# Kernel tuning notes

Measured on AMD Instinct MI355X. Metric: run time of the kernel, lower is better.

## Reference

```python
import jax, jax.numpy as jnp
import numpy as np

B, N, DIM = 2, 2048, 1024
H, DH = 16, 64
NNK = 2          # num_null_kv
SCALE = 8.0
LN_EPS = 1e-5
L2_EPS = 1e-12


def layer_norm(x, gamma):
    mu = jnp.mean(x, axis=-1, keepdims=True)
    var = jnp.var(x, axis=-1, keepdims=True)
    return (x - mu) * jax.lax.rsqrt(var + LN_EPS) * gamma  # beta buffer is zeros


def l2norm(t):
    n = jnp.sqrt(jnp.sum(t * t, axis=-1, keepdims=True))
    return t / jnp.maximum(n, L2_EPS)


def setup_inputs() -> dict:
    key = jax.random.key(0)
    ks = jax.random.split(key, 9)
    x = jax.random.normal(ks[0], (B, N, DIM), dtype=jnp.float32)
    mask = jax.random.randint(ks[1], (B, N), 0, 2).astype(bool)
    attn_bias = jax.random.normal(ks[2], (H, N, N), dtype=jnp.float32)
    gamma = jnp.ones((DIM,), dtype=jnp.float32)
    null_kv = jax.random.normal(ks[3], (H, 2 * NNK, DH), dtype=jnp.float32)
    Wq = jax.random.normal(ks[4], (DIM, H * DH), dtype=jnp.float32) * 0.02
    Wkv = jax.random.normal(ks[5], (DIM, 2 * H * DH), dtype=jnp.float32) * 0.02
    q_scale = jnp.ones((DH,), dtype=jnp.float32)
    k_scale = jnp.ones((DH,), dtype=jnp.float32)
    Wo = jax.random.normal(ks[6], (H * DH, DIM), dtype=jnp.float32) * 0.02
    return {"x": x, "mask": mask, "attn_bias": attn_bias, "gamma": gamma,
            "null_kv": null_kv, "Wq": Wq, "Wkv": Wkv,
            "q_scale": q_scale, "k_scale": k_scale, "Wo": Wo}


def reference(x, mask, attn_bias, gamma, null_kv, Wq, Wkv, q_scale, k_scale, Wo):
    b, n, dim = x.shape
    h, dh = null_kv.shape[0], null_kv.shape[-1]
    # NOTE: in the original module kv_input is captured BEFORE self.norm(x),
    # so k/v come from the un-normalized x (context=None path).
    kv_input = x
    xn = layer_norm(x, gamma)
    q = (xn @ Wq).reshape(b, n, h, dh).transpose(0, 2, 1, 3)          # b h n d
    kv = (kv_input @ Wkv).reshape(b, n, 2, h, dh)
    k = kv[:, :, 0].transpose(0, 2, 1, 3)                              # b h n d
    v = kv[:, :, 1].transpose(0, 2, 1, 3)                              # b h n d
    # null kv: 'h (n r) d -> h n r d', unbind r
    nkv = null_kv.reshape(h, NNK, 2, dh)
    nk = jnp.broadcast_to(nkv[:, :, 0][None], (b, h, NNK, dh))
    nv = jnp.broadcast_to(nkv[:, :, 1][None], (b, h, NNK, dh))
    k = jnp.concatenate([nk, k], axis=-2)                              # b h j d
    v = jnp.concatenate([nv, v], axis=-2)
    q = l2norm(q) * q_scale
    k = l2norm(k) * k_scale
    sim = jnp.einsum('bhid,bhjd->bhij', q, k) * SCALE                  # b h i j
    i, j = sim.shape[-2], sim.shape[-1]
    # attn_bias padded with num_null_kv zeros on the left of last dim
    bias = jnp.pad(attn_bias, ((0, 0), (0, 0), (NNK, 0)))
    sim = sim + bias[None]                                             # broadcast over batch
    neg = -jnp.finfo(sim.dtype).max
    # key padding mask, null kv always attendable
    m = jnp.pad(mask, ((0, 0), (NNK, 0)), constant_values=True)       # b j
    sim = jnp.where(m[:, None, None, :], sim, neg)
    # causal mask with diagonal offset j - i + 1 (null tokens always visible)
    causal = jnp.triu(jnp.ones((i, j), dtype=bool), k=j - i + 1)
    sim = jnp.where(causal, neg, sim)
    attn = jax.nn.softmax(sim, axis=-1)
    out = jnp.einsum('bhij,bhjd->bhid', attn, v)
    out = out.transpose(0, 2, 1, 3).reshape(b, n, h * dh)
    return out @ Wo
```

## Files before the change

kernel.cpp:

```cpp
#include <hip/hip_runtime.h>
#include <math.h>

typedef unsigned short ushort_t;
typedef __attribute__((ext_vector_type(8))) short bf16x8_t;
typedef __attribute__((ext_vector_type(4))) float floatx4;

typedef __attribute__((address_space(3))) unsigned int lds_uint;
typedef const __attribute__((address_space(1))) unsigned int glob_uint;

__device__ inline void gl_lds16(const ushort_t* g, ushort_t* l) {
    __builtin_amdgcn_global_load_lds((glob_uint*)g, (lds_uint*)l, 16, 0, 0);
}

__device__ inline float bf2f(ushort_t u) {
    return __uint_as_float(((unsigned int)u) << 16);
}
__device__ inline ushort_t f2bf(float f) {
    unsigned int u = __float_as_uint(f);
    unsigned int r = (u + 0x7fffu + ((u >> 16) & 1u)) >> 16;
    return (ushort_t)r;
}
__device__ inline float wave_sum(float v) {
    #pragma unroll
    for (int m = 1; m < 64; m <<= 1) v += __shfl_xor(v, m, 64);
    return v;
}

__global__ __launch_bounds__(256) void transpose_split(const float* __restrict__ W,
                                                       ushort_t* __restrict__ WTh,
                                                       ushort_t* __restrict__ WTl,
                                                       int K, int N) {
    __shared__ float t[32][33];
    int n0 = blockIdx.x * 32, k0 = blockIdx.y * 32;
    int tx = threadIdx.x, ty = threadIdx.y;
    for (int i = ty; i < 32; i += 8)
        t[i][tx] = W[(size_t)(k0 + i) * N + n0 + tx];
    __syncthreads();
    for (int i = ty; i < 32; i += 8) {
        float v = t[tx][i];
        ushort_t hv = f2bf(v);
        size_t o = (size_t)(n0 + i) * K + k0 + tx;
        WTh[o] = hv;
        WTl[o] = f2bf(v - bf2f(hv));
    }
}

__global__ __launch_bounds__(256) void ln_split(const float* __restrict__ x,
                                                const float* __restrict__ gamma,
                                                ushort_t* __restrict__ xnh,
                                                ushort_t* __restrict__ xnl,
                                                ushort_t* __restrict__ xh,
                                                ushort_t* __restrict__ xl) {
    int row = blockIdx.x, tid = threadIdx.x;
    int wid = tid >> 6, lane = tid & 63;
    float v[4];
    float s1 = 0.f, s2 = 0.f;
    #pragma unroll
    for (int i = 0; i < 4; ++i) {
        v[i] = x[(size_t)row * 1024 + tid + 256 * i];
        s1 += v[i];
        s2 += v[i] * v[i];
    }
    s1 = wave_sum(s1);
    s2 = wave_sum(s2);
    __shared__ float red[8];
    if (lane == 0) { red[wid] = s1; red[4 + wid] = s2; }
    __syncthreads();
    float S1 = red[0] + red[1] + red[2] + red[3];
    float S2 = red[4] + red[5] + red[6] + red[7];
    float mu = S1 * (1.0f / 1024.0f);
    float var = S2 * (1.0f / 1024.0f) - mu * mu;
    float rs = 1.0f / sqrtf(var + 1e-5f);
    #pragma unroll
    for (int i = 0; i < 4; ++i) {
        int c = tid + 256 * i;
        size_t o = (size_t)row * 1024 + c;
        ushort_t hx = f2bf(v[i]);
        xh[o] = hx;
        xl[o] = f2bf(v[i] - bf2f(hx));
        float xnv = (v[i] - mu) * rs * gamma[c];
        ushort_t hn = f2bf(xnv);
        xnh[o] = hn;
        xnl[o] = f2bf(xnv - bf2f(hn));
    }
}

__global__ __launch_bounds__(256) void gemm_bf3(const ushort_t* __restrict__ Ah,
                                                const ushort_t* __restrict__ Al,
                                                const ushort_t* __restrict__ Bh,
                                                const ushort_t* __restrict__ Bl,
                                                float* __restrict__ C,
                                                int M, int N, int K) {
    __shared__ ushort_t As[128 * 64];
    __shared__ ushort_t Bs[128 * 64];
    int tid = threadIdx.x;
    int w = tid >> 6, lane = tid & 63;
    int wm = w >> 1, wn = w & 1;
    int row0 = blockIdx.y * 128, col0 = blockIdx.x * 128;
    int l15 = lane & 15, l4 = lane >> 4;
    int rx = l15 & 7;
    floatx4 acc[4][4];
    #pragma unroll
    for (int i = 0; i < 4; ++i)
        #pragma unroll
        for (int j = 0; j < 4; ++j)
            #pragma unroll
            for (int v = 0; v < 4; ++v) acc[i][j][v] = 0.f;

    int nk = K >> 5;
    for (int kt = 0; kt < nk; ++kt) {
        __syncthreads();
        #pragma unroll
        for (int c = 0; c < 4; ++c) {
            int idx = c * 256 + tid;
            int r = idx >> 3, cl = idx & 7;
            int cg = cl ^ (r & 7);
            const ushort_t* ga = (cg < 4 ? Ah : Al)
                + (size_t)(row0 + r) * K + kt * 32 + (cg & 3) * 8;
            gl_lds16(ga, &As[(c * 256 + w * 64) * 8]);
            const ushort_t* gb = (cg < 4 ? Bh : Bl)
                + (size_t)(col0 + r) * K + kt * 32 + (cg & 3) * 8;
            gl_lds16(gb, &Bs[(c * 256 + w * 64) * 8]);
        }
        __syncthreads();
        bf16x8_t af_h[4], af_l[4], bf_h[4], bf_l[4];
        #pragma unroll
        for (int mi = 0; mi < 4; ++mi) {
            int r = wm * 64 + mi * 16 + l15;
            af_h[mi] = *(const bf16x8_t*)&As[(r * 8 + (l4 ^ rx)) * 8];
            af_l[mi] = *(const bf16x8_t*)&As[(r * 8 + ((4 + l4) ^ rx)) * 8];
        }
        #pragma unroll
        for (int ni = 0; ni < 4; ++ni) {
            int r = wn * 64 + ni * 16 + l15;
            bf_h[ni] = *(const bf16x8_t*)&Bs[(r * 8 + (l4 ^ rx)) * 8];
            bf_l[ni] = *(const bf16x8_t*)&Bs[(r * 8 + ((4 + l4) ^ rx)) * 8];
        }
        #pragma unroll
        for (int mi = 0; mi < 4; ++mi)
            #pragma unroll
            for (int ni = 0; ni < 4; ++ni) {
                acc[mi][ni] = __builtin_amdgcn_mfma_f32_16x16x32_bf16(
                    af_h[mi], bf_h[ni], acc[mi][ni], 0, 0, 0);
                acc[mi][ni] = __builtin_amdgcn_mfma_f32_16x16x32_bf16(
                    af_h[mi], bf_l[ni], acc[mi][ni], 0, 0, 0);
                acc[mi][ni] = __builtin_amdgcn_mfma_f32_16x16x32_bf16(
                    af_l[mi], bf_h[ni], acc[mi][ni], 0, 0, 0);
            }
    }
    #pragma unroll
    for (int mi = 0; mi < 4; ++mi)
        #pragma unroll
        for (int ni = 0; ni < 4; ++ni)
            #pragma unroll
            for (int v = 0; v < 4; ++v) {
                int rr = row0 + wm * 64 + mi * 16 + l4 * 4 + v;
                int cc = col0 + wn * 64 + ni * 16 + l15;
                C[(size_t)rr * N + cc] = acc[mi][ni][v];
            }
}

__global__ __launch_bounds__(256) void l2scale_q(const float* __restrict__ q,
                                                 const float* __restrict__ qs,
                                                 ushort_t* __restrict__ Qh,
                                                 ushort_t* __restrict__ Ql) {
    int rid = blockIdx.x * 4 + (threadIdx.x >> 6);
    int lane = threadIdx.x & 63;
    int h = rid & 15, n = (rid >> 4) & 2047, b = rid >> 15;
    float v = q[(size_t)rid * 64 + lane];
    float nrm = sqrtf(wave_sum(v * v));
    float qn = v / fmaxf(nrm, 1e-12f) * qs[lane] * 8.0f;
    size_t o = (((size_t)(b * 16 + h)) * 2048 + n) * 64 + lane;
    ushort_t hv = f2bf(qn);
    Qh[o] = hv;
    Ql[o] = f2bf(qn - bf2f(hv));
}

__global__ __launch_bounds__(256) void build_kv(const float* __restrict__ kv,
                                                const float* __restrict__ nullkv,
                                                const float* __restrict__ ks,
                                                ushort_t* __restrict__ Kh,
                                                ushort_t* __restrict__ Kl,
                                                ushort_t* __restrict__ VTh) {
    __shared__ ushort_t Vt[64][72];
    int tid = threadIdx.x;
    int w = tid >> 6, lane = tid & 63;
    int bh = blockIdx.y, b = bh >> 4, h = bh & 15;
    int j0 = blockIdx.x * 64;
    for (int jj = 0; jj < 16; ++jj) {
        int jl = w * 16 + jj;
        int j = j0 + jl;
        float kf = 0.f, vf = 0.f;
        if (j < 2) {
            kf = nullkv[(h * 4 + 2 * j) * 64 + lane];
            vf = nullkv[(h * 4 + 2 * j + 1) * 64 + lane];
        } else if (j < 2050) {
            int n = j - 2;
            size_t base = ((size_t)b * 2048 + n) * 2048;
            kf = kv[base + h * 64 + lane];
            vf = kv[base + 1024 + h * 64 + lane];
        }
        float nrm = sqrtf(wave_sum(kf * kf));
        float kn = (j < 2050) ? kf / fmaxf(nrm, 1e-12f) * ks[lane] : 0.f;
        size_t o = ((size_t)bh * 2112 + j) * 64 + lane;
        ushort_t khv = f2bf(kn);
        Kh[o] = khv;
        Kl[o] = f2bf(kn - bf2f(khv));
        Vt[jl][lane] = f2bf(vf);
    }
    __syncthreads();
    int d = tid >> 2, seg = tid & 3;
    ushort_t buf[16];
    #pragma unroll
    for (int e = 0; e < 16; ++e) buf[e] = Vt[seg * 16 + e][d];
    size_t o = ((size_t)bh * 64 + d) * 2112 + j0 + seg * 16;
    *(bf16x8_t*)&VTh[o]     = *(const bf16x8_t*)&buf[0];
    *(bf16x8_t*)&VTh[o + 8] = *(const bf16x8_t*)&buf[8];
}

__global__ __launch_bounds__(256) void attn_mfma(const ushort_t* __restrict__ Qh,
                                                 const ushort_t* __restrict__ Ql,
                                                 const ushort_t* __restrict__ Kh,
                                                 const ushort_t* __restrict__ Kl,
                                                 const ushort_t* __restrict__ VTh,
                                                 const float* __restrict__ bias,
                                                 const int* __restrict__ mask,
                                                 ushort_t* __restrict__ aoh,
                                                 ushort_t* __restrict__ aol) {
    __shared__ ushort_t Ks[2][64 * 128];
    __shared__ ushort_t Vs[2][64 * 64];
    __shared__ ushort_t Ps[4][16 * 72];

    int tid = threadIdx.x;
    int w = tid >> 6, lane = tid & 63;
    int quad = lane >> 4, l15 = lane & 15;
    int rx = l15 & 7;
    int qt = 31 - blockIdx.x;
    int bh = blockIdx.y;
    int b = bh >> 4, h = bh & 15;
    int i0 = qt * 64, r0 = i0 + w * 16;
    const int nIter = qt + 2;

    auto stage = [&](int j0, ushort_t* kd, ushort_t* vd) {
        #pragma unroll
        for (int c = 0; c < 4; ++c) {
            int idx = c * 256 + tid;
            int r = idx >> 4, cl = idx & 15;
            int cg = (cl & 8) | ((cl ^ (r & 7)) & 7);
            const ushort_t* g = ((cg & 8) ? Kl : Kh)
                + ((size_t)bh * 2112 + j0 + r) * 64 + (cg & 7) * 8;
            gl_lds16(g, &kd[(c * 256 + w * 64) * 8]);
        }
        #pragma unroll
        for (int c = 0; c < 2; ++c) {
            int idx = c * 256 + tid;
            int r = idx >> 3, cl = idx & 7;
            int cg = cl ^ (r & 7);
            const ushort_t* g = VTh + ((size_t)bh * 64 + r) * 2112 + j0 + cg * 8;
            gl_lds16(g, &vd[(c * 256 + w * 64) * 8]);
        }
    };

    float bv_n[4][4];
    int km_n[4];
    auto prefetchB = [&](int j0n) {
        #pragma unroll
        for (int jt = 0; jt < 4; ++jt) {
            int jg = j0n + jt * 16 + l15;
            km_n[jt] = (jg < 2) ? 1 : (jg < 2050 ? mask[b * 2048 + jg - 2] : 0);
            #pragma unroll
            for (int reg = 0; reg < 4; ++reg) {
                int ig = r0 + quad * 4 + reg;
                bv_n[jt][reg] = (jg >= 2 && jg < 2050)
                    ? bias[((size_t)h * 2048 + ig) * 2048 + (jg - 2)] : 0.f;
            }
        }
    };

    stage(0, Ks[0], Vs[0]);
    prefetchB(0);

    bf16x8_t aqh[2], aql[2];
    {
        size_t qbase = ((size_t)bh * 2048 + r0 + l15) * 64 + quad * 8;
        aqh[0] = *(const bf16x8_t*)&Qh[qbase];
        aqh[1] = *(const bf16x8_t*)&Qh[qbase + 32];
        aql[0] = *(const bf16x8_t*)&Ql[qbase];
        aql[1] = *(const bf16x8_t*)&Ql[qbase + 32];
    }

    floatx4 o_acc[4];
    float l_acc[4];
    #pragma unroll
    for (int dt = 0; dt < 4; ++dt)
        #pragma unroll
        for (int v = 0; v < 4; ++v) o_acc[dt][v] = 0.f;
    #pragma unroll
    for (int r = 0; r < 4; ++r) l_acc[r] = 0.f;

    __syncthreads();

    for (int it = 0; it < nIter; ++it) {
        int cur = it & 1;
        int j0 = it * 64;

        float bv[4][4];
        int km[4];
        #pragma unroll
        for (int jt = 0; jt < 4; ++jt) {
            km[jt] = km_n[jt];
            #pragma unroll
            for (int reg = 0; reg < 4; ++reg) bv[jt][reg] = bv_n[jt][reg];
        }
        if (it + 1 < nIter) {
            stage(j0 + 64, Ks[cur ^ 1], Vs[cur ^ 1]);
            prefetchB(j0 + 64);
        }
        const ushort_t* ks = Ks[cur];
        const ushort_t* vs = Vs[cur];

        floatx4 s_acc[4];
        #pragma unroll
        for (int jt = 0; jt < 4; ++jt) {
            floatx4 acc;
            #pragma unroll
            for (int v = 0; v < 4; ++v) acc[v] = 0.f;
            int r = jt * 16 + l15;
            #pragma unroll
            for (int ks2 = 0; ks2 < 2; ++ks2) {
                int cc = ks2 * 4 + quad;
                bf16x8_t kbh = *(const bf16x8_t*)&ks[(r * 16 + (cc ^ rx)) * 8];
                bf16x8_t kbl = *(const bf16x8_t*)&ks[(r * 16 + 8 + (cc ^ rx)) * 8];
                acc = __builtin_amdgcn_mfma_f32_16x16x32_bf16(aqh[ks2], kbh, acc, 0, 0, 0);
                acc = __builtin_amdgcn_mfma_f32_16x16x32_bf16(aql[ks2], kbh, acc, 0, 0, 0);
                acc = __builtin_amdgcn_mfma_f32_16x16x32_bf16(aqh[ks2], kbl, acc, 0, 0, 0);
            }
            s_acc[jt] = acc;
        }

        #pragma unroll
        for (int jt = 0; jt < 4; ++jt) {
            int jg = j0 + jt * 16 + l15;
            #pragma unroll
            for (int reg = 0; reg < 4; ++reg) {
                int ig = r0 + quad * 4 + reg;
                float sv = s_acc[jt][reg] + bv[jt][reg] - 16.0f;
                bool ok = (km[jt] != 0) && (jg <= ig + 2);
                float pv = ok ? __expf(sv) : 0.0f;
                l_acc[reg] += pv;
                Ps[w][(quad * 4 + reg) * 72 + jt * 16 + l15] = f2bf(pv);
            }
        }

        #pragma unroll
        for (int ks2 = 0; ks2 < 2; ++ks2) {
            bf16x8_t pf = *(const bf16x8_t*)&Ps[w][l15 * 72 + ks2 * 32 + quad * 8];
            #pragma unroll
            for (int dt = 0; dt < 4; ++dt) {
                int r = dt * 16 + l15;
                int cc = ks2 * 4 + quad;
                bf16x8_t vh = *(const bf16x8_t*)&vs[(r * 8 + (cc ^ rx)) * 8];
                o_acc[dt] = __builtin_amdgcn_mfma_f32_16x16x32_bf16(pf, vh, o_acc[dt], 0, 0, 0);
            }
        }

        __syncthreads();
    }

    #pragma unroll
    for (int reg = 0; reg < 4; ++reg) {
        #pragma unroll
        for (int m2 = 1; m2 < 16; m2 <<= 1)
            l_acc[reg] += __shfl_xor(l_acc[reg], m2, 64);
    }
    #pragma unroll
    for (int dt = 0; dt < 4; ++dt)
        #pragma unroll
        for (int reg = 0; reg < 4; ++reg) {
            int ig = r0 + quad * 4 + reg;
            float ov = o_acc[dt][reg] / l_acc[reg];
            size_t o = ((size_t)b * 2048 + ig) * 1024 + h * 64 + dt * 16 + l15;
            ushort_t hv = f2bf(ov);
            aoh[o] = hv;
            aol[o] = f2bf(ov - bf2f(hv));
        }
}

extern "C" void kernel_launch(void* const* d_in, const int* in_sizes, int n_in,
                              void* d_out, int out_size, void* d_ws, size_t ws_size,
                              hipStream_t stream) {
    const float* x         = (const float*)d_in[0];
    const int*   mask      = (const int*)d_in[1];
    const float* attn_bias = (const float*)d_in[2];
    const float* gamma     = (const float*)d_in[3];
    const float* null_kv   = (const float*)d_in[4];
    const float* Wq        = (const float*)d_in[5];
    const float* Wkv       = (const float*)d_in[6];
    const float* q_scale   = (const float*)d_in[7];
    const float* k_scale   = (const float*)d_in[8];
    const float* Wo        = (const float*)d_in[9];

    char* ws = (char*)d_ws;
    ushort_t* xnh   = (ushort_t*)ws; ws += (size_t)4096 * 1024 * 2;
    ushort_t* xnl   = (ushort_t*)ws; ws += (size_t)4096 * 1024 * 2;
    ushort_t* xh    = (ushort_t*)ws; ws += (size_t)4096 * 1024 * 2;
    ushort_t* xl    = (ushort_t*)ws; ws += (size_t)4096 * 1024 * 2;
    ushort_t* WqTh  = (ushort_t*)ws; ws += (size_t)1024 * 1024 * 2;
    ushort_t* WqTl  = (ushort_t*)ws; ws += (size_t)1024 * 1024 * 2;
    ushort_t* WkvTh = (ushort_t*)ws; ws += (size_t)2048 * 1024 * 2;
    ushort_t* WkvTl = (ushort_t*)ws; ws += (size_t)2048 * 1024 * 2;
    ushort_t* WoTh  = (ushort_t*)ws; ws += (size_t)1024 * 1024 * 2;
    ushort_t* WoTl  = (ushort_t*)ws; ws += (size_t)1024 * 1024 * 2;
    float*    q_ws  = (float*)ws;    ws += (size_t)4096 * 1024 * 4;
    float*    kvws  = (float*)ws;    ws += (size_t)4096 * 2048 * 4;
    ushort_t* Qh    = (ushort_t*)ws; ws += (size_t)32 * 2048 * 64 * 2;
    ushort_t* Ql    = (ushort_t*)ws; ws += (size_t)32 * 2048 * 64 * 2;
    ushort_t* Kh    = (ushort_t*)ws; ws += (size_t)32 * 2112 * 64 * 2;
    ushort_t* Kl    = (ushort_t*)ws; ws += (size_t)32 * 2112 * 64 * 2;
    ushort_t* VTh   = (ushort_t*)ws; ws += (size_t)32 * 2112 * 64 * 2;
    ushort_t* aoh   = (ushort_t*)ws; ws += (size_t)4096 * 1024 * 2;
    ushort_t* aol   = (ushort_t*)ws; ws += (size_t)4096 * 1024 * 2;

    transpose_split<<<dim3(32, 32), dim3(32, 8), 0, stream>>>(Wq, WqTh, WqTl, 1024, 1024);
    transpose_split<<<dim3(64, 32), dim3(32, 8), 0, stream>>>(Wkv, WkvTh, WkvTl, 1024, 2048);
    transpose_split<<<dim3(32, 32), dim3(32, 8), 0, stream>>>(Wo, WoTh, WoTl, 1024, 1024);
    ln_split<<<4096, 256, 0, stream>>>(x, gamma, xnh, xnl, xh, xl);
    gemm_bf3<<<dim3(8, 32), 256, 0, stream>>>(xnh, xnl, WqTh, WqTl, q_ws, 4096, 1024, 1024);
    gemm_bf3<<<dim3(16, 32), 256, 0, stream>>>(xh, xl, WkvTh, WkvTl, kvws, 4096, 2048, 1024);
    l2scale_q<<<16384, 256, 0, stream>>>(q_ws, q_scale, Qh, Ql);
    build_kv<<<dim3(33, 32), 256, 0, stream>>>(kvws, null_kv, k_scale, Kh, Kl, VTh);
    attn_mfma<<<dim3(32, 32), 256, 0, stream>>>(Qh, Ql, Kh, Kl, VTh, attn_bias, mask, aoh, aol);
    gemm_bf3<<<dim3(8, 32), 256, 0, stream>>>(aoh, aol, WoTh, WoTl, (float*)d_out, 4096, 1024, 1024);
}
```

Before: 683.1 us.

## Double-buffer GEMM LDS tiles and use 128x64 tiles for N=1024 GEMMs

Adds a second LDS buffer to the split-bf16 GEMM so the global-to-LDS load of the next K tile is issued before the MFMA work on the current tile, with one barrier per iteration instead of two. Adds a 128x64-tile variant and uses it for the Q and output projections, doubling their block count from 256 to 512 so the grid covers more CUs. The cost is twice the shared memory per block, which may lower occupancy, and less B-tile reuse in the narrower variant.

```diff
diff --git a/kernel.cpp b/kernel.cpp
--- a/kernel.cpp
+++ b/kernel.cpp
@@ -91,8 +91,8 @@
                                                 const ushort_t* __restrict__ Bl,
                                                 float* __restrict__ C,
                                                 int M, int N, int K) {
-    __shared__ ushort_t As[128 * 64];
-    __shared__ ushort_t Bs[128 * 64];
+    __shared__ ushort_t As[2][128 * 64];
+    __shared__ ushort_t Bs[2][128 * 64];
     int tid = threadIdx.x;
     int w = tid >> 6, lane = tid & 63;
     int wm = w >> 1, wn = w & 1;
@@ -107,9 +107,7 @@
             #pragma unroll
             for (int v = 0; v < 4; ++v) acc[i][j][v] = 0.f;
 
-    int nk = K >> 5;
-    for (int kt = 0; kt < nk; ++kt) {
-        __syncthreads();
+    auto stage = [&](int kt, int bufi) {
         #pragma unroll
         for (int c = 0; c < 4; ++c) {
             int idx = c * 256 + tid;
@@ -117,24 +115,31 @@
             int cg = cl ^ (r & 7);
             const ushort_t* ga = (cg < 4 ? Ah : Al)
                 + (size_t)(row0 + r) * K + kt * 32 + (cg & 3) * 8;
-            gl_lds16(ga, &As[(c * 256 + w * 64) * 8]);
+            gl_lds16(ga, &As[bufi][(c * 256 + w * 64) * 8]);
             const ushort_t* gb = (cg < 4 ? Bh : Bl)
                 + (size_t)(col0 + r) * K + kt * 32 + (cg & 3) * 8;
-            gl_lds16(gb, &Bs[(c * 256 + w * 64) * 8]);
-        }
-        __syncthreads();
+            gl_lds16(gb, &Bs[bufi][(c * 256 + w * 64) * 8]);
+        }
+    };
+
+    int nk = K >> 5;
+    stage(0, 0);
+    __syncthreads();
+    for (int kt = 0; kt < nk; ++kt) {
+        int cur = kt & 1;
+        if (kt + 1 < nk) stage(kt + 1, cur ^ 1);
         bf16x8_t af_h[4], af_l[4], bf_h[4], bf_l[4];
         #pragma unroll
         for (int mi = 0; mi < 4; ++mi) {
             int r = wm * 64 + mi * 16 + l15;
-            af_h[mi] = *(const bf16x8_t*)&As[(r * 8 + (l4 ^ rx)) * 8];
-            af_l[mi] = *(const bf16x8_t*)&As[(r * 8 + ((4 + l4) ^ rx)) * 8];
+            af_h[mi] = *(const bf16x8_t*)&As[cur][(r * 8 + (l4 ^ rx)) * 8];
+            af_l[mi] = *(const bf16x8_t*)&As[cur][(r * 8 + ((4 + l4) ^ rx)) * 8];
         }
         #pragma unroll
         for (int ni = 0; ni < 4; ++ni) {
             int r = wn * 64 + ni * 16 + l15;
-            bf_h[ni] = *(const bf16x8_t*)&Bs[(r * 8 + (l4 ^ rx)) * 8];
-            bf_l[ni] = *(const bf16x8_t*)&Bs[(r * 8 + ((4 + l4) ^ rx)) * 8];
+            bf_h[ni] = *(const bf16x8_t*)&Bs[cur][(r * 8 + (l4 ^ rx)) * 8];
+            bf_l[ni] = *(const bf16x8_t*)&Bs[cur][(r * 8 + ((4 + l4) ^ rx)) * 8];
         }
         #pragma unroll
         for (int mi = 0; mi < 4; ++mi)
@@ -147,6 +152,7 @@
                 acc[mi][ni] = __builtin_amdgcn_mfma_f32_16x16x32_bf16(
                     af_l[mi], bf_h[ni], acc[mi][ni], 0, 0, 0);
             }
+        __syncthreads();
     }
     #pragma unroll
     for (int mi = 0; mi < 4; ++mi)
@@ -156,6 +162,92 @@
             for (int v = 0; v < 4; ++v) {
                 int rr = row0 + wm * 64 + mi * 16 + l4 * 4 + v;
                 int cc = col0 + wn * 64 + ni * 16 + l15;
+                C[(size_t)rr * N + cc] = acc[mi][ni][v];
+            }
+}
+
+__global__ __launch_bounds__(256) void gemm_bf3_n64(const ushort_t* __restrict__ Ah,
+                                                    const ushort_t* __restrict__ Al,
+                                                    const ushort_t* __restrict__ Bh,
+                                                    const ushort_t* __restrict__ Bl,
+                                                    float* __restrict__ C,
+                                                    int M, int N, int K) {
+    __shared__ ushort_t As[2][128 * 64];
+    __shared__ ushort_t Bs[2][64 * 64];
+    int tid = threadIdx.x;
+    int w = tid >> 6, lane = tid & 63;
+    int row0 = blockIdx.y * 128, col0 = blockIdx.x * 64;
+    int l15 = lane & 15, l4 = lane >> 4;
+    int rx = l15 & 7;
+    floatx4 acc[2][4];
+    #pragma unroll
+    for (int i = 0; i < 2; ++i)
+        #pragma unroll
+        for (int j = 0; j < 4; ++j)
+            #pragma unroll
+            for (int v = 0; v < 4; ++v) acc[i][j][v] = 0.f;
+
+    auto stage = [&](int kt, int bufi) {
+        #pragma unroll
+        for (int c = 0; c < 4; ++c) {
+            int idx = c * 256 + tid;
+            int r = idx >> 3, cl = idx & 7;
+            int cg = cl ^ (r & 7);
+            const ushort_t* ga = (cg < 4 ? Ah : Al)
+                + (size_t)(row0 + r) * K + kt * 32 + (cg & 3) * 8;
+            gl_lds16(ga, &As[bufi][(c * 256 + w * 64) * 8]);
+        }
+        #pragma unroll
+        for (int c = 0; c < 2; ++c) {
+            int idx = c * 256 + tid;
+            int r = idx >> 3, cl = idx & 7;
+            int cg = cl ^ (r & 7);
+            const ushort_t* gb = (cg < 4 ? Bh : Bl)
+                + (size_t)(col0 + r) * K + kt * 32 + (cg & 3) * 8;
+            gl_lds16(gb, &Bs[bufi][(c * 256 + w * 64) * 8]);
+        }
+    };
+
+    int nk = K >> 5;
+    stage(0, 0);
+    __syncthreads();
+    for (int kt = 0; kt < nk; ++kt) {
+        int cur = kt & 1;
+        if (kt + 1 < nk) stage(kt + 1, cur ^ 1);
+        bf16x8_t af_h[2], af_l[2], bf_h[4], bf_l[4];
+        #pragma unroll
+        for (int mi = 0; mi < 2; ++mi) {
+            int r = w * 32 + mi * 16 + l15;
+            af_h[mi] = *(const bf16x8_t*)&As[cur][(r * 8 + (l4 ^ rx)) * 8];
+            af_l[mi] = *(const bf16x8_t*)&As[cur][(r * 8 + ((4 + l4) ^ rx)) * 8];
+        }
+        #pragma unroll
+        for (int ni = 0; ni < 4; ++ni) {
+            int r = ni * 16 + l15;
+            bf_h[ni] = *(const bf16x8_t*)&Bs[cur][(r * 8 + (l4 ^ rx)) * 8];
+            bf_l[ni] = *(const bf16x8_t*)&Bs[cur][(r * 8 + ((4 + l4) ^ rx)) * 8];
+        }
+        #pragma unroll
+        for (int mi = 0; mi < 2; ++mi)
+            #pragma unroll
+            for (int ni = 0; ni < 4; ++ni) {
+                acc[mi][ni] = __builtin_amdgcn_mfma_f32_16x16x32_bf16(
+                    af_h[mi], bf_h[ni], acc[mi][ni], 0, 0, 0);
+                acc[mi][ni] = __builtin_amdgcn_mfma_f32_16x16x32_bf16(
+                    af_h[mi], bf_l[ni], acc[mi][ni], 0, 0, 0);
+                acc[mi][ni] = __builtin_amdgcn_mfma_f32_16x16x32_bf16(
+                    af_l[mi], bf_h[ni], acc[mi][ni], 0, 0, 0);
+            }
+        __syncthreads();
+    }
+    #pragma unroll
+    for (int mi = 0; mi < 2; ++mi)
+        #pragma unroll
+        for (int ni = 0; ni < 4; ++ni)
+            #pragma unroll
+            for (int v = 0; v < 4; ++v) {
+                int rr = row0 + w * 32 + mi * 16 + l4 * 4 + v;
+                int cc = col0 + ni * 16 + l15;
                 C[(size_t)rr * N + cc] = acc[mi][ni][v];
             }
 }
@@ -425,10 +517,10 @@
     transpose_split<<<dim3(64, 32), dim3(32, 8), 0, stream>>>(Wkv, WkvTh, WkvTl, 1024, 2048);
     transpose_split<<<dim3(32, 32), dim3(32, 8), 0, stream>>>(Wo, WoTh, WoTl, 1024, 1024);
     ln_split<<<4096, 256, 0, stream>>>(x, gamma, xnh, xnl, xh, xl);
-    gemm_bf3<<<dim3(8, 32), 256, 0, stream>>>(xnh, xnl, WqTh, WqTl, q_ws, 4096, 1024, 1024);
+    gemm_bf3_n64<<<dim3(16, 32), 256, 0, stream>>>(xnh, xnl, WqTh, WqTl, q_ws, 4096, 1024, 1024);
     gemm_bf3<<<dim3(16, 32), 256, 0, stream>>>(xh, xl, WkvTh, WkvTl, kvws, 4096, 2048, 1024);
     l2scale_q<<<16384, 256, 0, stream>>>(q_ws, q_scale, Qh, Ql);
     build_kv<<<dim3(33, 32), 256, 0, stream>>>(kvws, null_kv, k_scale, Kh, Kl, VTh);
     attn_mfma<<<dim3(32, 32), 256, 0, stream>>>(Qh, Ql, Kh, Kl, VTh, attn_bias, mask, aoh, aol);
-    gemm_bf3<<<dim3(8, 32), 256, 0, stream>>>(aoh, aol, WoTh, WoTl, (float*)d_out, 4096, 1024, 1024);
-}
+    gemm_bf3_n64<<<dim3(16, 32), 256, 0, stream>>>(aoh, aol, WoTh, WoTl, (float*)d_out, 4096, 1024, 1024);
+}
```

Result: faster. 657.7 us (-3.7%).
